# Performance work log

Hardware: AMD Instinct MI355X
Metric: run time of the kernel (lower is better)

## Reference

```python
import jax, jax.numpy as jnp
import numpy as np

B, S, D, H = 2, 2048, 512, 8
DK = D // H


def setup_inputs() -> dict:
    key = jax.random.key(0)
    ks = jax.random.split(key, 6)
    q = jax.random.normal(ks[0], (B, S, D), dtype=jnp.float32)
    k = jax.random.normal(ks[1], (B, S, D), dtype=jnp.float32)
    v = jax.random.normal(ks[2], (B, S, D), dtype=jnp.float32)
    mask = jax.random.randint(ks[3], (1, 1, S, S), 0, 2, dtype=jnp.int32)
    # nn.Linear weights [out, in]; scaled like torch default init
    Wq = jax.random.normal(ks[4], (D, D), dtype=jnp.float32) / np.sqrt(D)
    Wo = jax.random.normal(ks[5], (D, D), dtype=jnp.float32) / np.sqrt(D)
    return {"q": q, "k": k, "v": v, "mask": mask, "Wq": Wq, "Wo": Wo}


def _split_heads(x):
    # [B,S,D] -> [B,H,S,DK]
    return x.reshape(B, S, H, DK).transpose(0, 2, 1, 3)


def reference(q, k, v, mask, Wq, Wo):
    # NOTE: original module applies Wq to q, k AND v (faithful to source bug)
    query = _split_heads(q @ Wq.T)
    key_ = _split_heads(k @ Wq.T)
    value = _split_heads(v @ Wq.T)
    scores = jnp.einsum("bhqd,bhkd->bhqk", query, key_) / np.sqrt(DK).astype(np.float32)
    # original uses masked_fill_(mask==0, 1e-09) BEFORE softmax (not -inf)
    scores = jnp.where(mask == 0, jnp.float32(1e-9), scores)
    attn = jax.nn.softmax(scores, axis=-1)  # dropout p=0.0 -> identity
    x = jnp.einsum("bhqk,bhkd->bhqd", attn, value)
    x = x.transpose(0, 2, 1, 3).reshape(B, S, D)
    return x @ Wo.T
```

## Files before the change

### kernel.cpp

```cpp
#include <hip/hip_runtime.h>
#include <hip/hip_bf16.h>
#include <stdint.h>

#define S_LEN 2048
#define D_MOD 512
#define N_H   8
#define D_K   64

typedef short v8s __attribute__((ext_vector_type(8)));
typedef short v4s __attribute__((ext_vector_type(4)));
typedef float v4f __attribute__((ext_vector_type(4)));

__device__ __forceinline__ short f2bf(float f) {
  union { float f; unsigned u; } a; a.f = f;
  unsigned u = a.u;
  u += 0x7fffu + ((u >> 16) & 1u);
  return (short)(u >> 16);
}
__device__ __forceinline__ short f2bfh(float f) {
  union { float f; unsigned u; } a; a.f = f;
  return (short)((a.u + 0x8000u) >> 16);
}

__device__ __forceinline__ v4f mfma16(v8s a, v8s b, v4f c) {
  return __builtin_amdgcn_mfma_f32_16x16x32_bf16(a, b, c, 0, 0, 0);
}
__device__ __forceinline__ v4f mfma16x16(v4s a, v4s b, v4f c) {
  return __builtin_amdgcn_mfma_f32_16x16x16bf16_1k(a, b, c, 0, 0, 0);
}

__global__ __launch_bounds__(256) void proj_kernel(
    const float* __restrict__ q, const float* __restrict__ k,
    const float* __restrict__ v, const float* __restrict__ Wq,
    const float* __restrict__ Wo, const int* __restrict__ mask,
    short* __restrict__ QP, short* __restrict__ KP, short* __restrict__ VT,
    short* __restrict__ Wob, unsigned long long* __restrict__ mp)
{
  const int z = blockIdx.z;
  const int tid = threadIdx.x;
  if (z == 3) {
    int bid = blockIdx.x * 8 + blockIdx.y;
    if (bid < 256) {
      int id = bid * 256 + tid;
      const int4* m4 = (const int4*)(mask + (size_t)id * 64);
      unsigned long long w = 0ull;
#pragma unroll
      for (int j = 0; j < 16; j++) {
        int4 mv = m4[j];
        w |= (unsigned long long)(mv.x != 0) << (j * 4 + 0);
        w |= (unsigned long long)(mv.y != 0) << (j * 4 + 1);
        w |= (unsigned long long)(mv.z != 0) << (j * 4 + 2);
        w |= (unsigned long long)(mv.w != 0) << (j * 4 + 3);
      }
      mp[id] = w;
    } else {
      unsigned off = (bid - 256) * 256 + tid;
      float4 x = ((const float4*)Wo)[off];
      v4s p; p.x = f2bf(x.x); p.y = f2bf(x.y); p.z = f2bf(x.z); p.w = f2bf(x.w);
      ((v4s*)Wob)[off] = p;
    }
    return;
  }
  const float* __restrict__ A = (z == 0) ? q : ((z == 1) ? k : v);
  const int m0 = blockIdx.x * 64, n0 = blockIdx.y * 64;
  const int wave = tid >> 6, lane = tid & 63;
  const int quad = lane >> 4, l15 = lane & 15;
  const int wm = wave >> 1, wn = wave & 1;
  __shared__ short As[64][72];
  __shared__ short Bs[64][72];
  v4f acc[2][2];
#pragma unroll
  for (int i = 0; i < 2; i++)
#pragma unroll
    for (int j = 0; j < 2; j++) acc[i][j] = (v4f){0.f, 0.f, 0.f, 0.f};

  float4 a4[4], b4[4];
#pragma unroll
  for (int i = 0; i < 4; i++) {
    int fi = tid + i * 256, r = fi >> 4, c = (fi & 15) << 2;
    a4[i] = *(const float4*)&A[(m0 + r) * 512 + c];
    b4[i] = *(const float4*)&Wq[(n0 + r) * 512 + c];
  }

  for (int kk = 0; kk < 512; kk += 64) {
    __syncthreads();
#pragma unroll
    for (int i = 0; i < 4; i++) {
      int fi = tid + i * 256, r = fi >> 4, c = (fi & 15) << 2;
      v4s ap; ap.x = f2bf(a4[i].x); ap.y = f2bf(a4[i].y); ap.z = f2bf(a4[i].z); ap.w = f2bf(a4[i].w);
      *(v4s*)&As[r][c] = ap;
      v4s bp; bp.x = f2bf(b4[i].x); bp.y = f2bf(b4[i].y); bp.z = f2bf(b4[i].z); bp.w = f2bf(b4[i].w);
      *(v4s*)&Bs[r][c] = bp;
    }
    __syncthreads();
    if (kk + 64 < 512) {
#pragma unroll
      for (int i = 0; i < 4; i++) {
        int fi = tid + i * 256, r = fi >> 4, c = (fi & 15) << 2;
        a4[i] = *(const float4*)&A[(m0 + r) * 512 + kk + 64 + c];
        b4[i] = *(const float4*)&Wq[(n0 + r) * 512 + kk + 64 + c];
      }
    }
#pragma unroll
    for (int ms = 0; ms < 2; ms++)
#pragma unroll
      for (int ns = 0; ns < 2; ns++)
#pragma unroll
        for (int ks = 0; ks < 2; ks++) {
          union { v8s v; v4s h2[2]; } a, bb;
          a.h2[0]  = *(const v4s*)&As[wm * 32 + ms * 16 + l15][ks * 32 + quad * 8];
          a.h2[1]  = *(const v4s*)&As[wm * 32 + ms * 16 + l15][ks * 32 + quad * 8 + 4];
          bb.h2[0] = *(const v4s*)&Bs[wn * 32 + ns * 16 + l15][ks * 32 + quad * 8];
          bb.h2[1] = *(const v4s*)&Bs[wn * 32 + ns * 16 + l15][ks * 32 + quad * 8 + 4];
          acc[ms][ns] = mfma16(a.v, bb.v, acc[ms][ns]);
        }
  }
#pragma unroll
  for (int ms = 0; ms < 2; ms++)
#pragma unroll
    for (int ns = 0; ns < 2; ns++) {
      int mb = m0 + wm * 32 + ms * 16 + quad * 4;
      int n  = n0 + wn * 32 + ns * 16 + l15;
      int bI = mb >> 11, s = mb & 2047, hh = n >> 6, dk = n & 63;
      if (z == 2) {
        v4s pv;
        pv.x = f2bf(acc[ms][ns][0]); pv.y = f2bf(acc[ms][ns][1]);
        pv.z = f2bf(acc[ms][ns][2]); pv.w = f2bf(acc[ms][ns][3]);
        *(v4s*)&VT[((bI * N_H + hh) * D_K + dk) * S_LEN + s] = pv;
      } else {
        short* dst = (z == 0) ? QP : KP;
#pragma unroll
        for (int r = 0; r < 4; r++)
          dst[((bI * N_H + hh) * S_LEN + (s + r)) * D_K + dk] = f2bf(acc[ms][ns][r]);
      }
    }
}

__global__ __launch_bounds__(512, 4) void attn_kernel(
    const short* __restrict__ QP, const short* __restrict__ KP,
    const short* __restrict__ VT, const unsigned long long* __restrict__ mp,
    short* __restrict__ XP)
{
  const int h = blockIdx.y, b = blockIdx.z;
  const int tid = threadIdx.x;
  const int wave = tid >> 6;
  const int grp  = wave >> 1;
  const int wg   = wave & 1;
  const int lane = tid & 63;
  const int quad = lane >> 4, l15 = lane & 15;
  const short* Qh = QP + ((b * N_H + h) * S_LEN) * D_K;
  const short* Kh = KP + ((b * N_H + h) * S_LEN) * D_K;
  const short* Vh = VT + ((b * N_H + h) * D_K) * S_LEN;

  __shared__ char smem[73728];
  short* Ks = (short*)smem + grp * 4608;
  short* Vs = (short*)(smem + 36864) + grp * 4608;
  float* CB = (float*)smem;

  const int qrow0 = blockIdx.x * 64 + wg * 32;
  const int t128 = tid & 127;
  const int srow = t128 >> 1;
  const int sc   = (t128 & 1) * 32;
  const int ck0  = grp * 512;

  v8s aQ[2][2];
#pragma unroll
  for (int g = 0; g < 2; g++)
#pragma unroll
    for (int ks = 0; ks < 2; ks++)
      aQ[g][ks] = *(const v8s*)&Qh[(qrow0 + g * 16 + l15) * D_K + ks * 32 + quad * 8];

  const float C1 = 0.18033688011112042f;
  const float C2 = -11.541560327111707f;
  const v4s ONES4 = {16256, 16256, 16256, 16256};
  v4f accX[2][4], accL[2];
#pragma unroll
  for (int g = 0; g < 2; g++) {
    accL[g] = (v4f){0.f, 0.f, 0.f, 0.f};
#pragma unroll
    for (int u = 0; u < 4; u++) accX[g][u] = (v4f){0.f, 0.f, 0.f, 0.f};
  }

  v8s kr[4], vr[4];
#pragma unroll
  for (int j = 0; j < 4; j++) {
    kr[j] = *(const v8s*)&Kh[(ck0 + srow) * D_K + sc + j * 8];
    vr[j] = *(const v8s*)&Vh[srow * S_LEN + ck0 + sc + j * 8];
  }
  unsigned long long mwc[2], mwn[2] = {0ull, 0ull};
#pragma unroll
  for (int g = 0; g < 2; g++)
    mwc[g] = mp[(qrow0 + g * 16 + l15) * 32 + grp * 8];

  for (int kt = 0; kt < 8; kt++) {
    __syncthreads();
#pragma unroll
    for (int j = 0; j < 4; j++) {
      *(v8s*)&Ks[srow * 72 + sc + j * 8] = kr[j];
      *(v8s*)&Vs[srow * 72 + sc + j * 8] = vr[j];
    }
    __syncthreads();

    if (kt + 1 < 8) {
      const int c1 = ck0 + (kt + 1) * 64;
#pragma unroll
      for (int j = 0; j < 4; j++) {
        kr[j] = *(const v8s*)&Kh[(c1 + srow) * D_K + sc + j * 8];
        vr[j] = *(const v8s*)&Vh[srow * S_LEN + c1 + sc + j * 8];
      }
#pragma unroll
      for (int g = 0; g < 2; g++)
        mwn[g] = mp[(qrow0 + g * 16 + l15) * 32 + grp * 8 + kt + 1];
    }

    v4s pa[2][4];
#pragma unroll
    for (int tp = 0; tp < 4; tp++) {
      v8s bK0 = *(const v8s*)&Ks[(tp * 16 + l15) * 72 + quad * 8];
      v8s bK1 = *(const v8s*)&Ks[(tp * 16 + l15) * 72 + 32 + quad * 8];
#pragma unroll
      for (int g = 0; g < 2; g++) {
        v4f s = mfma16(bK0, aQ[g][0], (v4f){0.f, 0.f, 0.f, 0.f});
        s = mfma16(bK1, aQ[g][1], s);
        unsigned mb = (unsigned)(mwc[g] >> (tp * 16 + quad * 4));
        v4s pk;
#pragma unroll
        for (int r = 0; r < 4; r++) {
          float se = ((mb >> r) & 1u) ? s[r] : 0.0f;
          float p = __builtin_amdgcn_exp2f(fmaf(se, C1, C2));
          pk[r] = f2bfh(p);
        }
        pa[g][tp] = pk;
      }
    }

#pragma unroll
    for (int u = 0; u < 4; u++) {
      const short* vb_ = &Vs[(u * 16 + l15) * 72 + quad * 4];
#pragma unroll
      for (int tp = 0; tp < 4; tp++) {
        v4s bV = *(const v4s*)&vb_[tp * 16];
        accX[0][u] = mfma16x16(pa[0][tp], bV, accX[0][u]);
        accX[1][u] = mfma16x16(pa[1][tp], bV, accX[1][u]);
      }
    }
#pragma unroll
    for (int g = 0; g < 2; g++)
#pragma unroll
      for (int tp = 0; tp < 4; tp++)
        accL[g] = mfma16x16(pa[g][tp], ONES4, accL[g]);

    mwc[0] = mwn[0]; mwc[1] = mwn[1];
  }

  __syncthreads();
  if (grp > 0) {
    float* c = CB + ((grp - 1) * 128 + t128) * 41;
#pragma unroll
    for (int g = 0; g < 2; g++) {
#pragma unroll
      for (int u = 0; u < 4; u++)
#pragma unroll
        for (int r = 0; r < 4; r++) c[(g * 4 + u) * 4 + r] = accX[g][u][r];
#pragma unroll
      for (int r = 0; r < 4; r++) c[32 + g * 4 + r] = accL[g][r];
    }
  }
  __syncthreads();
  if (grp == 0) {
#pragma unroll
    for (int w = 0; w < 3; w++) {
      const float* c = CB + (w * 128 + t128) * 41;
#pragma unroll
      for (int g = 0; g < 2; g++) {
#pragma unroll
        for (int u = 0; u < 4; u++)
#pragma unroll
          for (int r = 0; r < 4; r++) accX[g][u][r] += c[(g * 4 + u) * 4 + r];
#pragma unroll
        for (int r = 0; r < 4; r++) accL[g][r] += c[32 + g * 4 + r];
      }
    }
#pragma unroll
    for (int g = 0; g < 2; g++) {
      float inv[4];
#pragma unroll
      for (int r = 0; r < 4; r++) inv[r] = 1.0f / accL[g][r];
#pragma unroll
      for (int u = 0; u < 4; u++)
#pragma unroll
        for (int r = 0; r < 4; r++) {
          int srw = qrow0 + g * 16 + quad * 4 + r;
          XP[(b * S_LEN + srw) * D_MOD + h * D_K + u * 16 + l15] =
              f2bf(accX[g][u][r] * inv[r]);
        }
    }
  }
}

__global__ __launch_bounds__(256) void outproj_kernel(
    const short* __restrict__ XP, const short* __restrict__ Wob,
    float* __restrict__ out)
{
  const int m0 = blockIdx.x * 64, n0 = blockIdx.y * 64;
  const int tid = threadIdx.x;
  const int wave = tid >> 6, lane = tid & 63;
  const int quad = lane >> 4, l15 = lane & 15;
  const int wm = wave >> 1, wn = wave & 1;
  __shared__ short As[64][72];
  __shared__ short Bs[64][72];
  v4f acc[2][2];
#pragma unroll
  for (int i = 0; i < 2; i++)
#pragma unroll
    for (int j = 0; j < 2; j++) acc[i][j] = (v4f){0.f, 0.f, 0.f, 0.f};

  v8s a8[2], b8[2];
#pragma unroll
  for (int i = 0; i < 2; i++) {
    int fi = tid + i * 256, r = fi >> 3, c = (fi & 7) << 3;
    a8[i] = *(const v8s*)&XP[(m0 + r) * 512 + c];
    b8[i] = *(const v8s*)&Wob[(n0 + r) * 512 + c];
  }

  for (int kk = 0; kk < 512; kk += 64) {
    __syncthreads();
#pragma unroll
    for (int i = 0; i < 2; i++) {
      int fi = tid + i * 256, r = fi >> 3, c = (fi & 7) << 3;
      *(v8s*)&As[r][c] = a8[i];
      *(v8s*)&Bs[r][c] = b8[i];
    }
    __syncthreads();
    if (kk + 64 < 512) {
#pragma unroll
      for (int i = 0; i < 2; i++) {
        int fi = tid + i * 256, r = fi >> 3, c = (fi & 7) << 3;
        a8[i] = *(const v8s*)&XP[(m0 + r) * 512 + kk + 64 + c];
        b8[i] = *(const v8s*)&Wob[(n0 + r) * 512 + kk + 64 + c];
      }
    }
#pragma unroll
    for (int ms = 0; ms < 2; ms++)
#pragma unroll
      for (int ns = 0; ns < 2; ns++)
#pragma unroll
        for (int ks = 0; ks < 2; ks++) {
          union { v8s v; v4s h2[2]; } a, bb;
          a.h2[0]  = *(const v4s*)&As[wm * 32 + ms * 16 + l15][ks * 32 + quad * 8];
          a.h2[1]  = *(const v4s*)&As[wm * 32 + ms * 16 + l15][ks * 32 + quad * 8 + 4];
          bb.h2[0] = *(const v4s*)&Bs[wn * 32 + ns * 16 + l15][ks * 32 + quad * 8];
          bb.h2[1] = *(const v4s*)&Bs[wn * 32 + ns * 16 + l15][ks * 32 + quad * 8 + 4];
          acc[ms][ns] = mfma16(a.v, bb.v, acc[ms][ns]);
        }
  }
#pragma unroll
  for (int ms = 0; ms < 2; ms++)
#pragma unroll
    for (int ns = 0; ns < 2; ns++) {
      int n = n0 + wn * 32 + ns * 16 + l15;
#pragma unroll
      for (int r = 0; r < 4; r++) {
        int m = m0 + wm * 32 + ms * 16 + quad * 4 + r;
        out[m * 512 + n] = acc[ms][ns][r];
      }
    }
}

extern "C" void kernel_launch(void* const* d_in, const int* in_sizes, int n_in,
                              void* d_out, int out_size, void* d_ws, size_t ws_size,
                              hipStream_t stream) {
  const float* q  = (const float*)d_in[0];
  const float* k  = (const float*)d_in[1];
  const float* v  = (const float*)d_in[2];
  const int* mask = (const int*)d_in[3];
  const float* Wq = (const float*)d_in[4];
  const float* Wo = (const float*)d_in[5];
  float* out = (float*)d_out;
  char* ws = (char*)d_ws;
  short* QP = (short*)(ws);
  short* KP = (short*)(ws + (4u << 20));
  short* VT = (short*)(ws + (8u << 20));
  short* XP = (short*)(ws + (12u << 20));
  unsigned long long* MP = (unsigned long long*)(ws + (16u << 20));
  short* Wob = (short*)(ws + (16u << 20) + (512u << 10));

  proj_kernel<<<dim3(64, 8, 4), 256, 0, stream>>>(q, k, v, Wq, Wo, mask,
                                                  QP, KP, VT, Wob, MP);
  attn_kernel<<<dim3(32, N_H, 2), 512, 0, stream>>>(QP, KP, VT, MP, XP);
  outproj_kernel<<<dim3(64, 8, 1), 256, 0, stream>>>(XP, Wob, out);
}
```

Measured before the change: 151.9 us.

## Split attention key range across blocks and merge partials in output projection

The attention kernel no longer splits the key range across wave groups inside one 512-thread block with a shared-memory reduction. It now launches four times as many 256-thread blocks, each covering one key quarter, and writes unnormalized fp32 partial outputs and row sums to global workspace. The output-projection kernel sums the four partials, applies the reciprocal of the summed row sums, and converts to bf16 while staging its A tile. This removes the in-block reduction and raises block count for occupancy, at the cost of much more global traffic: 32 MB of fp32 partials written and re-read four times by each column tile of the output GEMM.

```diff
diff --git a/kernel.cpp b/kernel.cpp
--- a/kernel.cpp
+++ b/kernel.cpp
@@ -136,171 +136,123 @@
     }
 }
 
-__global__ __launch_bounds__(512, 4) void attn_kernel(
+__global__ __launch_bounds__(256, 5) void attn_kernel(
     const short* __restrict__ QP, const short* __restrict__ KP,
-    const short* __restrict__ VT, const unsigned long long* __restrict__ mp,
-    short* __restrict__ XP)
+    const short* __restrict__ VT, const unsigned long long* __restrict__ MP,
+    float* __restrict__ XF, float* __restrict__ LP)
 {
+  const int bx = blockIdx.x;
+  const int qt = bx & 31, qu = bx >> 5;
   const int h = blockIdx.y, b = blockIdx.z;
   const int tid = threadIdx.x;
-  const int wave = tid >> 6;
-  const int grp  = wave >> 1;
-  const int wg   = wave & 1;
-  const int lane = tid & 63;
+  const int wave = tid >> 6, lane = tid & 63;
   const int quad = lane >> 4, l15 = lane & 15;
   const short* Qh = QP + ((b * N_H + h) * S_LEN) * D_K;
   const short* Kh = KP + ((b * N_H + h) * S_LEN) * D_K;
   const short* Vh = VT + ((b * N_H + h) * D_K) * S_LEN;
 
-  __shared__ char smem[73728];
-  short* Ks = (short*)smem + grp * 4608;
-  short* Vs = (short*)(smem + 36864) + grp * 4608;
-  float* CB = (float*)smem;
-
-  const int qrow0 = blockIdx.x * 64 + wg * 32;
-  const int t128 = tid & 127;
-  const int srow = t128 >> 1;
-  const int sc   = (t128 & 1) * 32;
-  const int ck0  = grp * 512;
-
-  v8s aQ[2][2];
-#pragma unroll
-  for (int g = 0; g < 2; g++)
-#pragma unroll
-    for (int ks = 0; ks < 2; ks++)
-      aQ[g][ks] = *(const v8s*)&Qh[(qrow0 + g * 16 + l15) * D_K + ks * 32 + quad * 8];
+  __shared__ short Ks[64][72];
+  __shared__ short Vs[64][72];
+
+  const int qrow = qt * 64 + wave * 16;
+  const int srow = tid >> 2;
+  const int sc   = (tid & 3) * 16;
+  const int ck0  = qu * 512;
+
+  v8s aQ[2];
+#pragma unroll
+  for (int ks = 0; ks < 2; ks++)
+    aQ[ks] = *(const v8s*)&Qh[(qrow + l15) * D_K + ks * 32 + quad * 8];
 
   const float C1 = 0.18033688011112042f;
   const float C2 = -11.541560327111707f;
   const v4s ONES4 = {16256, 16256, 16256, 16256};
-  v4f accX[2][4], accL[2];
-#pragma unroll
-  for (int g = 0; g < 2; g++) {
-    accL[g] = (v4f){0.f, 0.f, 0.f, 0.f};
-#pragma unroll
-    for (int u = 0; u < 4; u++) accX[g][u] = (v4f){0.f, 0.f, 0.f, 0.f};
-  }
-
-  v8s kr[4], vr[4];
-#pragma unroll
-  for (int j = 0; j < 4; j++) {
+  v4f accX[4], accL = (v4f){0.f, 0.f, 0.f, 0.f};
+#pragma unroll
+  for (int u = 0; u < 4; u++) accX[u] = (v4f){0.f, 0.f, 0.f, 0.f};
+
+  v8s kr[2], vr[2];
+#pragma unroll
+  for (int j = 0; j < 2; j++) {
     kr[j] = *(const v8s*)&Kh[(ck0 + srow) * D_K + sc + j * 8];
     vr[j] = *(const v8s*)&Vh[srow * S_LEN + ck0 + sc + j * 8];
   }
-  unsigned long long mwc[2], mwn[2] = {0ull, 0ull};
-#pragma unroll
-  for (int g = 0; g < 2; g++)
-    mwc[g] = mp[(qrow0 + g * 16 + l15) * 32 + grp * 8];
+  unsigned long long mwc = MP[(qrow + l15) * 32 + qu * 8];
+  unsigned long long mwn = 0ull;
 
   for (int kt = 0; kt < 8; kt++) {
     __syncthreads();
 #pragma unroll
-    for (int j = 0; j < 4; j++) {
-      *(v8s*)&Ks[srow * 72 + sc + j * 8] = kr[j];
-      *(v8s*)&Vs[srow * 72 + sc + j * 8] = vr[j];
+    for (int j = 0; j < 2; j++) {
+      *(v8s*)&Ks[srow][sc + j * 8] = kr[j];
+      *(v8s*)&Vs[srow][sc + j * 8] = vr[j];
     }
     __syncthreads();
 
     if (kt + 1 < 8) {
       const int c1 = ck0 + (kt + 1) * 64;
 #pragma unroll
-      for (int j = 0; j < 4; j++) {
+      for (int j = 0; j < 2; j++) {
         kr[j] = *(const v8s*)&Kh[(c1 + srow) * D_K + sc + j * 8];
         vr[j] = *(const v8s*)&Vh[srow * S_LEN + c1 + sc + j * 8];
       }
-#pragma unroll
-      for (int g = 0; g < 2; g++)
-        mwn[g] = mp[(qrow0 + g * 16 + l15) * 32 + grp * 8 + kt + 1];
-    }
-
-    v4s pa[2][4];
+      mwn = MP[(qrow + l15) * 32 + qu * 8 + kt + 1];
+    }
+
+    v4s pa[4];
 #pragma unroll
     for (int tp = 0; tp < 4; tp++) {
-      v8s bK0 = *(const v8s*)&Ks[(tp * 16 + l15) * 72 + quad * 8];
-      v8s bK1 = *(const v8s*)&Ks[(tp * 16 + l15) * 72 + 32 + quad * 8];
-#pragma unroll
-      for (int g = 0; g < 2; g++) {
-        v4f s = mfma16(bK0, aQ[g][0], (v4f){0.f, 0.f, 0.f, 0.f});
-        s = mfma16(bK1, aQ[g][1], s);
-        unsigned mb = (unsigned)(mwc[g] >> (tp * 16 + quad * 4));
-        v4s pk;
-#pragma unroll
-        for (int r = 0; r < 4; r++) {
-          float se = ((mb >> r) & 1u) ? s[r] : 0.0f;
-          float p = __builtin_amdgcn_exp2f(fmaf(se, C1, C2));
-          pk[r] = f2bfh(p);
-        }
-        pa[g][tp] = pk;
-      }
+      v8s bK0 = *(const v8s*)&Ks[tp * 16 + l15][quad * 8];
+      v8s bK1 = *(const v8s*)&Ks[tp * 16 + l15][32 + quad * 8];
+      v4f s = mfma16(bK0, aQ[0], (v4f){0.f, 0.f, 0.f, 0.f});
+      s = mfma16(bK1, aQ[1], s);
+      unsigned mb = (unsigned)(mwc >> (tp * 16 + quad * 4));
+      v4s pk;
+#pragma unroll
+      for (int r = 0; r < 4; r++) {
+        float se = ((mb >> r) & 1u) ? s[r] : 0.0f;
+        float p = __builtin_amdgcn_exp2f(fmaf(se, C1, C2));
+        pk[r] = f2bfh(p);
+      }
+      pa[tp] = pk;
     }
 
 #pragma unroll
     for (int u = 0; u < 4; u++) {
-      const short* vb_ = &Vs[(u * 16 + l15) * 72 + quad * 4];
+      const short* vb_ = &Vs[u * 16 + l15][quad * 4];
 #pragma unroll
       for (int tp = 0; tp < 4; tp++) {
         v4s bV = *(const v4s*)&vb_[tp * 16];
-        accX[0][u] = mfma16x16(pa[0][tp], bV, accX[0][u]);
-        accX[1][u] = mfma16x16(pa[1][tp], bV, accX[1][u]);
-      }
-    }
-#pragma unroll
-    for (int g = 0; g < 2; g++)
-#pragma unroll
-      for (int tp = 0; tp < 4; tp++)
-        accL[g] = mfma16x16(pa[g][tp], ONES4, accL[g]);
-
-    mwc[0] = mwn[0]; mwc[1] = mwn[1];
-  }
-
-  __syncthreads();
-  if (grp > 0) {
-    float* c = CB + ((grp - 1) * 128 + t128) * 41;
-#pragma unroll
-    for (int g = 0; g < 2; g++) {
-#pragma unroll
-      for (int u = 0; u < 4; u++)
-#pragma unroll
-        for (int r = 0; r < 4; r++) c[(g * 4 + u) * 4 + r] = accX[g][u][r];
-#pragma unroll
-      for (int r = 0; r < 4; r++) c[32 + g * 4 + r] = accL[g][r];
-    }
-  }
-  __syncthreads();
-  if (grp == 0) {
-#pragma unroll
-    for (int w = 0; w < 3; w++) {
-      const float* c = CB + (w * 128 + t128) * 41;
-#pragma unroll
-      for (int g = 0; g < 2; g++) {
-#pragma unroll
-        for (int u = 0; u < 4; u++)
-#pragma unroll
-          for (int r = 0; r < 4; r++) accX[g][u][r] += c[(g * 4 + u) * 4 + r];
-#pragma unroll
-        for (int r = 0; r < 4; r++) accL[g][r] += c[32 + g * 4 + r];
-      }
-    }
-#pragma unroll
-    for (int g = 0; g < 2; g++) {
-      float inv[4];
-#pragma unroll
-      for (int r = 0; r < 4; r++) inv[r] = 1.0f / accL[g][r];
-#pragma unroll
-      for (int u = 0; u < 4; u++)
-#pragma unroll
-        for (int r = 0; r < 4; r++) {
-          int srw = qrow0 + g * 16 + quad * 4 + r;
-          XP[(b * S_LEN + srw) * D_MOD + h * D_K + u * 16 + l15] =
-              f2bf(accX[g][u][r] * inv[r]);
-        }
+        accX[u] = mfma16x16(pa[tp], bV, accX[u]);
+      }
+    }
+#pragma unroll
+    for (int tp = 0; tp < 4; tp++)
+      accL = mfma16x16(pa[tp], ONES4, accL);
+
+    mwc = mwn;
+  }
+
+  float* xq = XF + (size_t)qu * 2097152u;
+#pragma unroll
+  for (int u = 0; u < 4; u++)
+#pragma unroll
+    for (int r = 0; r < 4; r++) {
+      int srw = qrow + quad * 4 + r;
+      xq[(b * S_LEN + srw) * D_MOD + h * D_K + u * 16 + l15] = accX[u][r];
+    }
+  if (l15 == 0) {
+#pragma unroll
+    for (int r = 0; r < 4; r++) {
+      int srw = qrow + quad * 4 + r;
+      LP[((qu * 2 + b) * S_LEN + srw) * N_H + h] = accL[r];
     }
   }
 }
 
 __global__ __launch_bounds__(256) void outproj_kernel(
-    const short* __restrict__ XP, const short* __restrict__ Wob,
-    float* __restrict__ out)
+    const float* __restrict__ XF, const float* __restrict__ LP,
+    const short* __restrict__ Wob, float* __restrict__ out)
 {
   const int m0 = blockIdx.x * 64, n0 = blockIdx.y * 64;
   const int tid = threadIdx.x;
@@ -309,26 +261,57 @@
   const int wm = wave >> 1, wn = wave & 1;
   __shared__ short As[64][72];
   __shared__ short Bs[64][72];
+  __shared__ float Linv[64][8];
+
+#pragma unroll
+  for (int i = 0; i < 2; i++) {
+    int e = tid + i * 256;
+    int rr = e >> 3, hh = e & 7;
+    int s = m0 + rr, bb = s >> 11, sl = s & 2047;
+    float l = 0.f;
+#pragma unroll
+    for (int qu = 0; qu < 4; qu++)
+      l += LP[((qu * 2 + bb) * S_LEN + sl) * N_H + hh];
+    Linv[rr][hh] = 1.0f / l;
+  }
+
   v4f acc[2][2];
 #pragma unroll
   for (int i = 0; i < 2; i++)
 #pragma unroll
     for (int j = 0; j < 2; j++) acc[i][j] = (v4f){0.f, 0.f, 0.f, 0.f};
 
-  v8s a8[2], b8[2];
+  float af[2][8];
+  v8s b8[2];
 #pragma unroll
   for (int i = 0; i < 2; i++) {
     int fi = tid + i * 256, r = fi >> 3, c = (fi & 7) << 3;
-    a8[i] = *(const v8s*)&XP[(m0 + r) * 512 + c];
+    size_t base = (size_t)(m0 + r) * 512 + c;
+    float4 s0 = *(const float4*)&XF[base];
+    float4 s1 = *(const float4*)&XF[base + 4];
+#pragma unroll
+    for (int qu = 1; qu < 4; qu++) {
+      const float* p = XF + (size_t)qu * 2097152u + base;
+      float4 t0 = *(const float4*)p;
+      float4 t1 = *(const float4*)(p + 4);
+      s0.x += t0.x; s0.y += t0.y; s0.z += t0.z; s0.w += t0.w;
+      s1.x += t1.x; s1.y += t1.y; s1.z += t1.z; s1.w += t1.w;
+    }
+    af[i][0] = s0.x; af[i][1] = s0.y; af[i][2] = s0.z; af[i][3] = s0.w;
+    af[i][4] = s1.x; af[i][5] = s1.y; af[i][6] = s1.z; af[i][7] = s1.w;
     b8[i] = *(const v8s*)&Wob[(n0 + r) * 512 + c];
   }
+  __syncthreads();
 
   for (int kk = 0; kk < 512; kk += 64) {
-    __syncthreads();
 #pragma unroll
     for (int i = 0; i < 2; i++) {
       int fi = tid + i * 256, r = fi >> 3, c = (fi & 7) << 3;
-      *(v8s*)&As[r][c] = a8[i];
+      float inv = Linv[r][kk >> 6];
+      v8s ap;
+#pragma unroll
+      for (int j = 0; j < 8; j++) ap[j] = f2bf(af[i][j] * inv);
+      *(v8s*)&As[r][c] = ap;
       *(v8s*)&Bs[r][c] = b8[i];
     }
     __syncthreads();
@@ -336,7 +319,19 @@
 #pragma unroll
       for (int i = 0; i < 2; i++) {
         int fi = tid + i * 256, r = fi >> 3, c = (fi & 7) << 3;
-        a8[i] = *(const v8s*)&XP[(m0 + r) * 512 + kk + 64 + c];
+        size_t base = (size_t)(m0 + r) * 512 + kk + 64 + c;
+        float4 s0 = *(const float4*)&XF[base];
+        float4 s1 = *(const float4*)&XF[base + 4];
+#pragma unroll
+        for (int qu = 1; qu < 4; qu++) {
+          const float* p = XF + (size_t)qu * 2097152u + base;
+          float4 t0 = *(const float4*)p;
+          float4 t1 = *(const float4*)(p + 4);
+          s0.x += t0.x; s0.y += t0.y; s0.z += t0.z; s0.w += t0.w;
+          s1.x += t1.x; s1.y += t1.y; s1.z += t1.z; s1.w += t1.w;
+        }
+        af[i][0] = s0.x; af[i][1] = s0.y; af[i][2] = s0.z; af[i][3] = s0.w;
+        af[i][4] = s1.x; af[i][5] = s1.y; af[i][6] = s1.z; af[i][7] = s1.w;
         b8[i] = *(const v8s*)&Wob[(n0 + r) * 512 + kk + 64 + c];
       }
     }
@@ -353,6 +348,7 @@
           bb.h2[1] = *(const v4s*)&Bs[wn * 32 + ns * 16 + l15][ks * 32 + quad * 8 + 4];
           acc[ms][ns] = mfma16(a.v, bb.v, acc[ms][ns]);
         }
+    __syncthreads();
   }
 #pragma unroll
   for (int ms = 0; ms < 2; ms++)
@@ -381,12 +377,13 @@
   short* QP = (short*)(ws);
   short* KP = (short*)(ws + (4u << 20));
   short* VT = (short*)(ws + (8u << 20));
-  short* XP = (short*)(ws + (12u << 20));
   unsigned long long* MP = (unsigned long long*)(ws + (16u << 20));
   short* Wob = (short*)(ws + (16u << 20) + (512u << 10));
+  float* XF = (float*)(ws + (17u << 20));
+  float* LP = (float*)(ws + (49u << 20));
 
   proj_kernel<<<dim3(64, 8, 4), 256, 0, stream>>>(q, k, v, Wq, Wo, mask,
                                                   QP, KP, VT, Wob, MP);
-  attn_kernel<<<dim3(32, N_H, 2), 512, 0, stream>>>(QP, KP, VT, MP, XP);
-  outproj_kernel<<<dim3(64, 8, 1), 256, 0, stream>>>(XP, Wob, out);
-}
+  attn_kernel<<<dim3(128, N_H, 2), 256, 0, stream>>>(QP, KP, VT, MP, XF, LP);
+  outproj_kernel<<<dim3(64, 8, 1), 256, 0, stream>>>(XF, LP, Wob, out);
+}
```

New measurement: 158.4 us. 4.3% more time.
